# Kernel optimization log

Measured on AMD Instinct MI355X. Metric: run time of the kernel, lower is better.

Reference implementation:

```python
import jax, jax.numpy as jnp
import numpy as np

E, IN, H1, H2, H3, A, B = 20, 512, 1024, 512, 256, 32, 4096


def setup_inputs() -> dict:
    key = jax.random.key(0)
    ks = jax.random.split(key, 10)

    def w(k, shape, fan_in):
        return jax.random.normal(k, shape, dtype=jnp.float32) / np.sqrt(fan_in)

    return {
        "obs": jax.random.normal(ks[0], (B, IN), dtype=jnp.float32),
        # stacked expert MLP params [E, ...]
        "eW1": w(ks[1], (E, IN, H1), IN), "eb1": jnp.zeros((E, H1), jnp.float32),
        "eW2": w(ks[2], (E, H1, H2), H1), "eb2": jnp.zeros((E, H2), jnp.float32),
        "eW3": w(ks[3], (E, H2, H3), H2), "eb3": jnp.zeros((E, H3), jnp.float32),
        "eW4": w(ks[4], (E, H3, A), H3), "eb4": jnp.zeros((E, A), jnp.float32),
        # gate MLP params
        "gW1": w(ks[5], (IN, H1), IN), "gb1": jnp.zeros((H1,), jnp.float32),
        "gW2": w(ks[6], (H1, H2), H1), "gb2": jnp.zeros((H2,), jnp.float32),
        "gW3": w(ks[7], (H2, H3), H2), "gb3": jnp.zeros((H3,), jnp.float32),
        "gW4": w(ks[8], (H3, E), H3), "gb4": jnp.zeros((E,), jnp.float32),
    }


def _experts(obs, eW1, eb1, eW2, eb2, eW3, eb3, eW4, eb4):
    # batched over experts: [B, E, h]
    h = jax.nn.elu(jnp.einsum('bi,eih->beh', obs, eW1) + eb1[None])
    h = jax.nn.elu(jnp.einsum('beh,ehk->bek', h, eW2) + eb2[None])
    h = jax.nn.elu(jnp.einsum('bek,ekm->bem', h, eW3) + eb3[None])
    return jnp.einsum('bem,ema->bea', h, eW4) + eb4[None]  # [B, E, A]


def _gate(obs, gW1, gb1, gW2, gb2, gW3, gb3, gW4, gb4):
    h = jax.nn.elu(obs @ gW1 + gb1)
    h = jax.nn.elu(h @ gW2 + gb2)
    h = jax.nn.elu(h @ gW3 + gb3)
    return jax.nn.softmax(h @ gW4 + gb4, axis=-1)  # [B, E]


def reference(obs, eW1, eb1, eW2, eb2, eW3, eb3, eW4, eb4,
              gW1, gb1, gW2, gb2, gW3, gb3, gW4, gb4):
    weights = _gate(obs, gW1, gb1, gW2, gb2, gW3, gb3, gW4, gb4)       # [B, E]
    actions = _experts(obs, eW1, eb1, eW2, eb2, eW3, eb3, eW4, eb4)    # [B, E, A]
    # bmm(weights[:,None,:], actions).squeeze(1)
    return jnp.einsum('be,bea->ba', weights, actions)                   # [B, A]
```

## Files before the change

### kernel.cpp

```cpp
#include <hip/hip_runtime.h>

#define B_SZ 4096
#define E_EXP 20
#define NE 21

typedef unsigned short u16;
typedef __bf16 bf16x8 __attribute__((ext_vector_type(8)));
typedef u16 u16x8 __attribute__((ext_vector_type(8)));
typedef u16 u16x4 __attribute__((ext_vector_type(4)));
typedef float floatx4 __attribute__((ext_vector_type(4)));

static __device__ __forceinline__ u16 f2bf(float f) {
  unsigned u = __builtin_bit_cast(unsigned, f);
  u += 0x7fffu + ((u >> 16) & 1u);
  return (u16)(u >> 16);
}

static __device__ __forceinline__ float elu1(float v) {
  return v > 0.f ? v : (__expf(v) - 1.f);
}

static __device__ __forceinline__ bf16x8 ld_bf8(const u16* p) {
  u16x8 v = *reinterpret_cast<const u16x8*>(p);
  return __builtin_bit_cast(bf16x8, v);
}

static __device__ __forceinline__ void gld_lds16(const u16* g, u16* l) {
  __builtin_amdgcn_global_load_lds(
      (const __attribute__((address_space(1))) unsigned int*)g,
      (__attribute__((address_space(3))) unsigned int*)l, 16, 0, 0);
}


__global__ void convert_obs_kernel(const float* __restrict__ src,
                                   u16* __restrict__ dst, int n) {
  int i = (blockIdx.x * blockDim.x + threadIdx.x) * 4;
  if (i < n) {
    float4 v = *reinterpret_cast<const float4*>(src + i);
    u16x4 o;
    o.x = f2bf(v.x); o.y = f2bf(v.y); o.z = f2bf(v.z); o.w = f2bf(v.w);
    *reinterpret_cast<u16x4*>(dst + i) = o;
  }
}

__global__ void transpose_conv_kernel(const float* __restrict__ src_e,
                                      const float* __restrict__ src_g,
                                      int n_e, int K, int N, int Nout,
                                      u16* __restrict__ dst) {
  int e = blockIdx.z;
  const float* src = (e < n_e) ? (src_e + (long)e * K * N) : src_g;
  __shared__ float tile[32][33];
  int tx = threadIdx.x & 31;
  int ty = threadIdx.x >> 5;
  int kbase = blockIdx.x * 32;
  int nbase = blockIdx.y * 32;
#pragma unroll
  for (int i = 0; i < 4; ++i) {
    int k = kbase + ty + i * 8;
    int n = nbase + tx;
    float v = 0.f;
    if (k < K && n < N) v = src[(long)k * N + n];
    tile[ty + i * 8][tx] = v;
  }
  __syncthreads();
  u16* dstE = dst + (long)e * Nout * K;
#pragma unroll
  for (int i = 0; i < 4; ++i) {
    int n = nbase + ty + i * 8;
    int k = kbase + tx;
    if (n < Nout && k < K) dstE[(long)n * K + k] = f2bf(tile[tx][ty + i * 8]);
  }
}

__global__ void concat_bias_kernel(const float* __restrict__ e_b,
                                   const float* __restrict__ g_b,
                                   int E, int H, float* __restrict__ dst) {
  int i = blockIdx.x * blockDim.x + threadIdx.x;
  int total = (E + 1) * H;
  if (i < total) dst[i] = (i < E * H) ? e_b[i] : g_b[i - E * H];
}


#define BM 128
#define BN 128

__global__ __launch_bounds__(256) void gemm_bias_elu_kernel(
    const u16* __restrict__ A_base, long a_estride,
    const u16* __restrict__ Wt_base, long w_estride,
    const float* __restrict__ bias_base, long b_estride,
    u16* __restrict__ C_base, long c_estride,
    int M, int N, int K) {
  int e = blockIdx.z;
  const u16* A = A_base + (long)e * a_estride;
  const u16* Wt = Wt_base + (long)e * w_estride;
  const float* bias = bias_base + (long)e * b_estride;
  u16* C = C_base + (long)e * c_estride;

  int m0 = blockIdx.y * BM;
  int n0 = blockIdx.x * BN;

  __shared__ u16 As[2 * BM * 32];
  __shared__ u16 Bs[2 * BN * 32];

  int tid = threadIdx.x;
  int lane = tid & 63;
  int w = tid >> 6;
  int wm = (w >> 1) * 64;
  int wn = (w & 1) * 64;
  int col = lane & 15;
  int quad = lane >> 4;

  floatx4 acc[4][4] = {};

  int srow = tid >> 2;
  int scol = (tid & 3) * 8;
  const u16* gA0 = &A[(long)(m0 + srow) * K + scol];
  const u16* gA1 = gA0 + (long)64 * K;
  const u16* gB0 = &Wt[(long)(n0 + srow) * K + scol];
  const u16* gB1 = gB0 + (long)64 * K;

  for (int k0 = 0; k0 < K; k0 += 64) {
    __syncthreads();
    gld_lds16(gA0 + k0, &As[(size_t)tid * 8]);
    gld_lds16(gA1 + k0, &As[(size_t)(256 + tid) * 8]);
    gld_lds16(gA0 + k0 + 32, &As[(size_t)(512 + tid) * 8]);
    gld_lds16(gA1 + k0 + 32, &As[(size_t)(768 + tid) * 8]);
    gld_lds16(gB0 + k0, &Bs[(size_t)tid * 8]);
    gld_lds16(gB1 + k0, &Bs[(size_t)(256 + tid) * 8]);
    gld_lds16(gB0 + k0 + 32, &Bs[(size_t)(512 + tid) * 8]);
    gld_lds16(gB1 + k0 + 32, &Bs[(size_t)(768 + tid) * 8]);
    __syncthreads();

#pragma unroll
    for (int kk = 0; kk < 2; ++kk) {
      bf16x8 xf[4], wf[4];
#pragma unroll
      for (int t = 0; t < 4; ++t) {
        xf[t] = __builtin_bit_cast(bf16x8,
            *reinterpret_cast<u16x8*>(
                &As[kk * BM * 32 + (wm + t * 16 + col) * 32 + quad * 8]));
        wf[t] = __builtin_bit_cast(bf16x8,
            *reinterpret_cast<u16x8*>(
                &Bs[kk * BN * 32 + (wn + t * 16 + col) * 32 + quad * 8]));
      }
#pragma unroll
      for (int i = 0; i < 4; ++i)
#pragma unroll
        for (int j = 0; j < 4; ++j)
          acc[i][j] = __builtin_amdgcn_mfma_f32_16x16x32_bf16(
              wf[j], xf[i], acc[i][j], 0, 0, 0);
    }
  }

#pragma unroll
  for (int j = 0; j < 4; ++j) {
    int nn = n0 + wn + j * 16 + quad * 4;
    float4 b4 = *reinterpret_cast<const float4*>(&bias[nn]);
#pragma unroll
    for (int i = 0; i < 4; ++i) {
      int m = m0 + wm + i * 16 + col;
      u16x4 o;
      o.x = f2bf(elu1(acc[i][j][0] + b4.x));
      o.y = f2bf(elu1(acc[i][j][1] + b4.y));
      o.z = f2bf(elu1(acc[i][j][2] + b4.z));
      o.w = f2bf(elu1(acc[i][j][3] + b4.w));
      *reinterpret_cast<u16x4*>(&C[(long)m * N + nn]) = o;
    }
  }
}

__global__ __launch_bounds__(64) void final_combine_kernel(
    const u16* __restrict__ h3, const u16* __restrict__ W4t,
    const u16* __restrict__ gW4t, const float* __restrict__ eb4,
    const float* __restrict__ gb4, float* __restrict__ out) {
  const int H3 = 256;
  int lane = threadIdx.x;
  int col = lane & 15;
  int quad = lane >> 4;
  int r0 = blockIdx.x * 16;

  floatx4 g0 = {}, g1 = {};
  const u16* h3g = h3 + (long)E_EXP * B_SZ * H3;
#pragma unroll
  for (int k0 = 0; k0 < 256; k0 += 32) {
    bf16x8 a = ld_bf8(&h3g[(long)(r0 + col) * H3 + k0 + quad * 8]);
    bf16x8 b0 = ld_bf8(&gW4t[(long)col * H3 + k0 + quad * 8]);
    bf16x8 b1 = ld_bf8(&gW4t[(long)(16 + col) * H3 + k0 + quad * 8]);
    g0 = __builtin_amdgcn_mfma_f32_16x16x32_bf16(a, b0, g0, 0, 0, 0);
    g1 = __builtin_amdgcn_mfma_f32_16x16x32_bf16(a, b1, g1, 0, 0, 0);
  }

  float w0[4], w1[4];
  float gbc0 = gb4[col];
  float gbc1 = (col < 4) ? gb4[16 + col] : 0.f;
#pragma unroll
  for (int r = 0; r < 4; ++r) {
    float v0 = g0[r] + gbc0;
    float v1 = (col < 4) ? (g1[r] + gbc1) : -1e30f;
    float m = fmaxf(v0, v1);
#pragma unroll
    for (int s = 1; s < 16; s <<= 1) m = fmaxf(m, __shfl_xor(m, s, 64));
    float e0 = __expf(v0 - m);
    float e1 = (col < 4) ? __expf(v1 - m) : 0.f;
    float ssum = e0 + e1;
#pragma unroll
    for (int s = 1; s < 16; s <<= 1) ssum += __shfl_xor(ssum, s, 64);
    w0[r] = e0 / ssum;
    w1[r] = e1 / ssum;
  }

  floatx4 o0 = {}, o1 = {};
  for (int e = 0; e < E_EXP; ++e) {
    floatx4 a0 = {}, a1 = {};
    const u16* he = h3 + (long)e * B_SZ * H3;
    const u16* we = W4t + (long)e * 32 * H3;
#pragma unroll
    for (int k0 = 0; k0 < 256; k0 += 32) {
      bf16x8 a = ld_bf8(&he[(long)(r0 + col) * H3 + k0 + quad * 8]);
      bf16x8 b0 = ld_bf8(&we[(long)col * H3 + k0 + quad * 8]);
      bf16x8 b1 = ld_bf8(&we[(long)(16 + col) * H3 + k0 + quad * 8]);
      a0 = __builtin_amdgcn_mfma_f32_16x16x32_bf16(a, b0, a0, 0, 0, 0);
      a1 = __builtin_amdgcn_mfma_f32_16x16x32_bf16(a, b1, a1, 0, 0, 0);
    }
    float be0 = eb4[e * 32 + col];
    float be1 = eb4[e * 32 + 16 + col];
    int src = (lane & 48) + (e & 15);
#pragma unroll
    for (int r = 0; r < 4; ++r) {
      float wr = __shfl((e < 16) ? w0[r] : w1[r], src, 64);
      o0[r] += wr * (a0[r] + be0);
      o1[r] += wr * (a1[r] + be1);
    }
  }
#pragma unroll
  for (int r = 0; r < 4; ++r) {
    int row = r0 + quad * 4 + r;
    out[(long)row * 32 + col] = o0[r];
    out[(long)row * 32 + 16 + col] = o1[r];
  }
}


static inline size_t align256(size_t x) { return (x + 255) & ~(size_t)255; }

extern "C" void kernel_launch(void* const* d_in, const int* in_sizes, int n_in,
                              void* d_out, int out_size, void* d_ws,
                              size_t ws_size, hipStream_t stream) {
  const float* obs = (const float*)d_in[0];
  const float* eW1 = (const float*)d_in[1];
  const float* eb1 = (const float*)d_in[2];
  const float* eW2 = (const float*)d_in[3];
  const float* eb2 = (const float*)d_in[4];
  const float* eW3 = (const float*)d_in[5];
  const float* eb3 = (const float*)d_in[6];
  const float* eW4 = (const float*)d_in[7];
  const float* eb4 = (const float*)d_in[8];
  const float* gW1 = (const float*)d_in[9];
  const float* gb1 = (const float*)d_in[10];
  const float* gW2 = (const float*)d_in[11];
  const float* gb2 = (const float*)d_in[12];
  const float* gW3 = (const float*)d_in[13];
  const float* gb3 = (const float*)d_in[14];
  const float* gW4 = (const float*)d_in[15];
  const float* gb4 = (const float*)d_in[16];
  float* out = (float*)d_out;
  char* ws = (char*)d_ws;

  size_t off = 0;
  size_t OFF_OBS = off;  off = align256(off + (size_t)B_SZ * 512 * 2);
  size_t OFF_W1T = off;  off = align256(off + (size_t)NE * 1024 * 512 * 2);
  size_t OFF_W2T = off;  off = align256(off + (size_t)NE * 512 * 1024 * 2);
  size_t OFF_W3T = off;  off = align256(off + (size_t)NE * 256 * 512 * 2);
  size_t OFF_W4T = off;  off = align256(off + (size_t)E_EXP * 32 * 256 * 2);
  size_t OFF_GW4T = off; off = align256(off + (size_t)32 * 256 * 2);
  size_t OFF_B1 = off;   off = align256(off + (size_t)NE * 1024 * 4);
  size_t OFF_B2 = off;   off = align256(off + (size_t)NE * 512 * 4);
  size_t OFF_B3 = off;   off = align256(off + (size_t)NE * 256 * 4);
  size_t OFF_H3 = off;   off = align256(off + (size_t)NE * B_SZ * 256 * 2);

  int chunk = B_SZ;
  size_t OFF_H1 = off;
  while (chunk > 512) {
    size_t need = (size_t)NE * chunk * 1024 * 2 + (size_t)NE * chunk * 512 * 2;
    if (OFF_H1 + need <= ws_size) break;
    chunk >>= 1;
  }
  size_t OFF_H2 = align256(OFF_H1 + (size_t)NE * chunk * 1024 * 2);

  u16* obs_bf = (u16*)(ws + OFF_OBS);
  u16* W1t = (u16*)(ws + OFF_W1T);
  u16* W2t = (u16*)(ws + OFF_W2T);
  u16* W3t = (u16*)(ws + OFF_W3T);
  u16* W4t = (u16*)(ws + OFF_W4T);
  u16* gW4t = (u16*)(ws + OFF_GW4T);
  float* b1 = (float*)(ws + OFF_B1);
  float* b2 = (float*)(ws + OFF_B2);
  float* b3 = (float*)(ws + OFF_B3);
  u16* h3 = (u16*)(ws + OFF_H3);
  u16* h1 = (u16*)(ws + OFF_H1);
  u16* h2 = (u16*)(ws + OFF_H2);

  convert_obs_kernel<<<(B_SZ * 512 / 4 + 255) / 256, 256, 0, stream>>>(
      obs, obs_bf, B_SZ * 512);
  transpose_conv_kernel<<<dim3(16, 32, NE), 256, 0, stream>>>(
      eW1, gW1, E_EXP, 512, 1024, 1024, W1t);
  transpose_conv_kernel<<<dim3(32, 16, NE), 256, 0, stream>>>(
      eW2, gW2, E_EXP, 1024, 512, 512, W2t);
  transpose_conv_kernel<<<dim3(16, 8, NE), 256, 0, stream>>>(
      eW3, gW3, E_EXP, 512, 256, 256, W3t);
  transpose_conv_kernel<<<dim3(8, 1, E_EXP), 256, 0, stream>>>(
      eW4, nullptr, E_EXP, 256, 32, 32, W4t);
  transpose_conv_kernel<<<dim3(8, 1, 1), 256, 0, stream>>>(
      gW4, nullptr, 1, 256, 20, 32, gW4t);
  concat_bias_kernel<<<(NE * 1024 + 255) / 256, 256, 0, stream>>>(
      eb1, gb1, E_EXP, 1024, b1);
  concat_bias_kernel<<<(NE * 512 + 255) / 256, 256, 0, stream>>>(
      eb2, gb2, E_EXP, 512, b2);
  concat_bias_kernel<<<(NE * 256 + 255) / 256, 256, 0, stream>>>(
      eb3, gb3, E_EXP, 256, b3);

  for (int bc = 0; bc < B_SZ; bc += chunk) {
    gemm_bias_elu_kernel<<<dim3(1024 / BN, chunk / BM, NE), 256, 0, stream>>>(
        obs_bf + (size_t)bc * 512, 0L,
        W1t, (long)1024 * 512,
        b1, 1024L,
        h1, (long)chunk * 1024, chunk, 1024, 512);
    gemm_bias_elu_kernel<<<dim3(512 / BN, chunk / BM, NE), 256, 0, stream>>>(
        h1, (long)chunk * 1024,
        W2t, (long)512 * 1024,
        b2, 512L,
        h2, (long)chunk * 512, chunk, 512, 1024);
    gemm_bias_elu_kernel<<<dim3(256 / BN, chunk / BM, NE), 256, 0, stream>>>(
        h2, (long)chunk * 512,
        W3t, (long)256 * 512,
        b3, 256L,
        h3 + (size_t)bc * 256, (long)B_SZ * 256, chunk, 256, 512);
  }

  final_combine_kernel<<<B_SZ / 16, 64, 0, stream>>>(h3, W4t, gW4t, eb4, gb4,
                                                     out);
}
```

Before: 567.2 us.

## Vectorize weight transpose, merge bias concat kernels, split final combine across four waves

The weight transpose-convert kernel now uses 64x64 tiles with float4 global loads and 16-byte bf16 stores, so fewer blocks move more data each. The three bias concatenation launches are merged into one kernel to cut launch overhead. The final combine kernel now runs four waves per block, each handling a strided subset of experts, with partial outputs reduced through shared memory. This adds per-expert parallelism in the tail kernel, at the cost of recomputing the gate softmax in every wave and adding a block barrier.

```diff
diff --git a/kernel.cpp b/kernel.cpp
--- a/kernel.cpp
+++ b/kernel.cpp
@@ -43,43 +43,69 @@
   }
 }
 
-__global__ void transpose_conv_kernel(const float* __restrict__ src_e,
-                                      const float* __restrict__ src_g,
-                                      int n_e, int K, int N, int Nout,
-                                      u16* __restrict__ dst) {
+__global__ __launch_bounds__(256) void transpose_conv_kernel(
+    const float* __restrict__ src_e, const float* __restrict__ src_g,
+    int n_e, int K, int N, int Nout, u16* __restrict__ dst) {
   int e = blockIdx.z;
   const float* src = (e < n_e) ? (src_e + (long)e * K * N) : src_g;
-  __shared__ float tile[32][33];
-  int tx = threadIdx.x & 31;
-  int ty = threadIdx.x >> 5;
-  int kbase = blockIdx.x * 32;
-  int nbase = blockIdx.y * 32;
-#pragma unroll
-  for (int i = 0; i < 4; ++i) {
-    int k = kbase + ty + i * 8;
-    int n = nbase + tx;
-    float v = 0.f;
-    if (k < K && n < N) v = src[(long)k * N + n];
-    tile[ty + i * 8][tx] = v;
+  __shared__ float t[64][65];
+  int tid = threadIdx.x;
+  int kbase = blockIdx.x * 64;
+  int nbase = blockIdx.y * 64;
+
+  int kk = tid >> 4;
+  int n4 = (tid & 15) * 4;
+#pragma unroll
+  for (int p = 0; p < 4; ++p) {
+    int k = kbase + p * 16 + kk;
+    int n = nbase + n4;
+    float4 v = make_float4(0.f, 0.f, 0.f, 0.f);
+    if (n + 3 < N) {
+      v = *reinterpret_cast<const float4*>(&src[(long)k * N + n]);
+    } else {
+      float* vp = &v.x;
+      for (int j = 0; j < 4; ++j)
+        if (n + j < N) vp[j] = src[(long)k * N + n + j];
+    }
+    t[p * 16 + kk][n4 + 0] = v.x;
+    t[p * 16 + kk][n4 + 1] = v.y;
+    t[p * 16 + kk][n4 + 2] = v.z;
+    t[p * 16 + kk][n4 + 3] = v.w;
   }
   __syncthreads();
+
   u16* dstE = dst + (long)e * Nout * K;
-#pragma unroll
-  for (int i = 0; i < 4; ++i) {
-    int n = nbase + ty + i * 8;
-    int k = kbase + tx;
-    if (n < Nout && k < K) dstE[(long)n * K + k] = f2bf(tile[tx][ty + i * 8]);
-  }
-}
-
-__global__ void concat_bias_kernel(const float* __restrict__ e_b,
-                                   const float* __restrict__ g_b,
-                                   int E, int H, float* __restrict__ dst) {
+  int kk8 = (tid & 7) * 8;
+#pragma unroll
+  for (int p = 0; p < 2; ++p) {
+    int ln = p * 32 + (tid >> 3);
+    int n = nbase + ln;
+    if (n < Nout) {
+      u16x8 o;
+#pragma unroll
+      for (int j = 0; j < 8; ++j) o[j] = f2bf(t[kk8 + j][ln]);
+      *reinterpret_cast<u16x8*>(&dstE[(long)n * K + kbase + kk8]) = o;
+    }
+  }
+}
+
+__global__ void concat_bias3_kernel(
+    const float* __restrict__ eb1, const float* __restrict__ gb1,
+    const float* __restrict__ eb2, const float* __restrict__ gb2,
+    const float* __restrict__ eb3, const float* __restrict__ gb3,
+    float* __restrict__ b1, float* __restrict__ b2, float* __restrict__ b3) {
   int i = blockIdx.x * blockDim.x + threadIdx.x;
-  int total = (E + 1) * H;
-  if (i < total) dst[i] = (i < E * H) ? e_b[i] : g_b[i - E * H];
-}
-
+  const int S1 = NE * 1024, S2 = NE * 512, S3 = NE * 256;
+  if (i < S1) {
+    b1[i] = (i < E_EXP * 1024) ? eb1[i] : gb1[i - E_EXP * 1024];
+  } else if (i < S1 + S2) {
+    int j = i - S1;
+    b2[j] = (j < E_EXP * 512) ? eb2[j] : gb2[j - E_EXP * 512];
+  } else if (i < S1 + S2 + S3) {
+    int j = i - S1 - S2;
+    b3[j] = (j < E_EXP * 256) ? eb3[j] : gb3[j - E_EXP * 256];
+  }
+}
 
 #define BM 128
 #define BN 128
@@ -169,12 +195,14 @@
   }
 }
 
-__global__ __launch_bounds__(64) void final_combine_kernel(
+__global__ __launch_bounds__(256) void final_combine_kernel(
     const u16* __restrict__ h3, const u16* __restrict__ W4t,
     const u16* __restrict__ gW4t, const float* __restrict__ eb4,
     const float* __restrict__ gb4, float* __restrict__ out) {
   const int H3 = 256;
-  int lane = threadIdx.x;
+  int tid = threadIdx.x;
+  int lane = tid & 63;
+  int w = tid >> 6;
   int col = lane & 15;
   int quad = lane >> 4;
   int r0 = blockIdx.x * 16;
@@ -210,7 +238,7 @@
   }
 
   floatx4 o0 = {}, o1 = {};
-  for (int e = 0; e < E_EXP; ++e) {
+  for (int e = w; e < E_EXP; e += 4) {
     floatx4 a0 = {}, a1 = {};
     const u16* he = h3 + (long)e * B_SZ * H3;
     const u16* we = W4t + (long)e * 32 * H3;
@@ -232,11 +260,30 @@
       o1[r] += wr * (a1[r] + be1);
     }
   }
-#pragma unroll
-  for (int r = 0; r < 4; ++r) {
-    int row = r0 + quad * 4 + r;
-    out[(long)row * 32 + col] = o0[r];
-    out[(long)row * 32 + 16 + col] = o1[r];
+
+  __shared__ float red[3][64][8];
+  if (w > 0) {
+#pragma unroll
+    for (int r = 0; r < 4; ++r) {
+      red[w - 1][lane][r] = o0[r];
+      red[w - 1][lane][4 + r] = o1[r];
+    }
+  }
+  __syncthreads();
+  if (w == 0) {
+#pragma unroll
+    for (int ww = 0; ww < 3; ++ww)
+#pragma unroll
+      for (int r = 0; r < 4; ++r) {
+        o0[r] += red[ww][lane][r];
+        o1[r] += red[ww][lane][4 + r];
+      }
+#pragma unroll
+    for (int r = 0; r < 4; ++r) {
+      int row = r0 + quad * 4 + r;
+      out[(long)row * 32 + col] = o0[r];
+      out[(long)row * 32 + 16 + col] = o1[r];
+    }
   }
 }
 
@@ -302,22 +349,18 @@
 
   convert_obs_kernel<<<(B_SZ * 512 / 4 + 255) / 256, 256, 0, stream>>>(
       obs, obs_bf, B_SZ * 512);
-  transpose_conv_kernel<<<dim3(16, 32, NE), 256, 0, stream>>>(
+  transpose_conv_kernel<<<dim3(8, 16, NE), 256, 0, stream>>>(
       eW1, gW1, E_EXP, 512, 1024, 1024, W1t);
-  transpose_conv_kernel<<<dim3(32, 16, NE), 256, 0, stream>>>(
+  transpose_conv_kernel<<<dim3(16, 8, NE), 256, 0, stream>>>(
       eW2, gW2, E_EXP, 1024, 512, 512, W2t);
-  transpose_conv_kernel<<<dim3(16, 8, NE), 256, 0, stream>>>(
+  transpose_conv_kernel<<<dim3(8, 4, NE), 256, 0, stream>>>(
       eW3, gW3, E_EXP, 512, 256, 256, W3t);
-  transpose_conv_kernel<<<dim3(8, 1, E_EXP), 256, 0, stream>>>(
+  transpose_conv_kernel<<<dim3(4, 1, E_EXP), 256, 0, stream>>>(
       eW4, nullptr, E_EXP, 256, 32, 32, W4t);
-  transpose_conv_kernel<<<dim3(8, 1, 1), 256, 0, stream>>>(
+  transpose_conv_kernel<<<dim3(4, 1, 1), 256, 0, stream>>>(
       gW4, nullptr, 1, 256, 20, 32, gW4t);
-  concat_bias_kernel<<<(NE * 1024 + 255) / 256, 256, 0, stream>>>(
-      eb1, gb1, E_EXP, 1024, b1);
-  concat_bias_kernel<<<(NE * 512 + 255) / 256, 256, 0, stream>>>(
-      eb2, gb2, E_EXP, 512, b2);
-  concat_bias_kernel<<<(NE * 256 + 255) / 256, 256, 0, stream>>>(
-      eb3, gb3, E_EXP, 256, b3);
+  concat_bias3_kernel<<<(NE * 1792 + 255) / 256, 256, 0, stream>>>(
+      eb1, gb1, eb2, gb2, eb3, gb3, b1, b2, b3);
 
   for (int bc = 0; bc < B_SZ; bc += chunk) {
     gemm_bias_elu_kernel<<<dim3(1024 / BN, chunk / BM, NE), 256, 0, stream>>>(
@@ -337,6 +380,6 @@
         h3 + (size_t)bc * 256, (long)B_SZ * 256, chunk, 256, 512);
   }
 
-  final_combine_kernel<<<B_SZ / 16, 64, 0, stream>>>(h3, W4t, gW4t, eb4, gb4,
-                                                     out);
-}
+  final_combine_kernel<<<B_SZ / 16, 256, 0, stream>>>(h3, W4t, gW4t, eb4, gb4,
+                                                      out);
+}
```

Measured after the change: 551.4 us. 1.03x faster.
